# Kernel optimization log

Measured on AMD Instinct MI355X. Metric: run time of the kernel, lower is better.

Reference implementation:

```python
import jax, jax.numpy as jnp
import numpy as np

H = 64            # LSTM hidden size
EH = 2 * H        # encoder output feature dim (bidirectional, 128)
B, T = 512, 512


def setup_inputs() -> dict:
    key = jax.random.key(0)
    ks = jax.random.split(key, 16)
    s = 0.05
    inp = {
        "h0": jax.random.normal(ks[0], (2, B, H), jnp.float32),
        "c0": jax.random.normal(ks[1], (2, B, H), jnp.float32),
        "encoder_outputs": jax.random.normal(ks[2], (B, T, EH), jnp.float32),
        # attn: Linear(4*H=256 -> 1)
        "W_attn": jax.random.normal(ks[3], (1, 4 * H), jnp.float32) * s,
        "b_attn": jax.random.normal(ks[4], (1,), jnp.float32) * s,
        # attn_combine: Linear(256 -> 64)
        "W_comb": jax.random.normal(ks[5], (H, 4 * H), jnp.float32) * s,
        "b_comb": jax.random.normal(ks[6], (H,), jnp.float32) * s,
        # bidirectional LSTM (1 layer), PyTorch gate order i,f,g,o
        "w_ih_f": jax.random.normal(ks[7], (4 * H, H), jnp.float32) * s,
        "w_hh_f": jax.random.normal(ks[8], (4 * H, H), jnp.float32) * s,
        "b_ih_f": jax.random.normal(ks[9], (4 * H,), jnp.float32) * s,
        "b_hh_f": jax.random.normal(ks[10], (4 * H,), jnp.float32) * s,
        "w_ih_r": jax.random.normal(ks[11], (4 * H, H), jnp.float32) * s,
        "w_hh_r": jax.random.normal(ks[12], (4 * H, H), jnp.float32) * s,
        "b_ih_r": jax.random.normal(ks[13], (4 * H,), jnp.float32) * s,
        "b_hh_r": jax.random.normal(ks[14], (4 * H,), jnp.float32) * s,
        "di": 256,
    }
    return inp


def _lstm_cell(x, h, c, w_ih, w_hh, b_ih, b_hh):
    # x,h,c: (b, H); weights: (4H, H). PyTorch gate order: i, f, g, o.
    gates = x @ w_ih.T + b_ih + h @ w_hh.T + b_hh  # (b, 4H)
    i, f, g, o = jnp.split(gates, 4, axis=-1)
    c_new = jax.nn.sigmoid(f) * c + jax.nn.sigmoid(i) * jnp.tanh(g)
    h_new = jax.nn.sigmoid(o) * jnp.tanh(c_new)
    return h_new, c_new


def reference(h0, c0, encoder_outputs, W_attn, b_attn, W_comb, b_comb,
              w_ih_f, w_hh_f, b_ih_f, b_hh_f, w_ih_r, w_hh_r, b_ih_r, b_hh_r, di):
    b, t, h = encoder_outputs.shape
    # hidden[0].view(-1, 128): row-major flatten of (2,b,64) into (b,128)
    dec_hidden = h0.reshape(-1, 2 * H)  # (b, 128)
    hid_rep = jnp.broadcast_to(dec_hidden[:, None, :], (b, t, 2 * H))
    cat = jnp.concatenate([encoder_outputs, hid_rep], axis=2)  # (b,t,256)
    scores = cat @ W_attn.T + b_attn                 # (b,t,1)
    attn_w = jax.nn.softmax(scores, axis=1)          # softmax over time
    # bmm(enc^T (b,h,t), attn_w (b,t,1)) -> (b,h)
    attn_applied = jnp.einsum('bth,bt->bh', encoder_outputs, attn_w[..., 0])
    out = jnp.concatenate([encoder_outputs[:, di, :], attn_applied], axis=1)  # (b,256)
    out = jax.nn.relu(out @ W_comb.T + b_comb)       # (b,64)
    # single-step bidirectional LSTM (seq len 1: both directions see same step)
    h_f, c_f = _lstm_cell(out, h0[0], c0[0], w_ih_f, w_hh_f, b_ih_f, b_hh_f)
    h_r, c_r = _lstm_cell(out, h0[1], c0[1], w_ih_r, w_hh_r, b_ih_r, b_hh_r)
    output = jnp.concatenate([h_f, h_r], axis=-1)[:, None, :]  # (b,1,128)
    h_new = jnp.stack([h_f, h_r], axis=0)  # (2,b,64)
    c_new = jnp.stack([c_f, c_r], axis=0)
    return output, h_new, c_new
```

## Files before the change

kernel.cpp:

```cpp
#include <hip/hip_runtime.h>

#define B_  512
#define T_  512
#define H_  64
#define EH_ 128
#define NW  8
#define NG  32

__device__ __forceinline__ float sigm(float x) { return 1.0f / (1.0f + __expf(-x)); }

__device__ __forceinline__ float dot4(const float4& a, const float4& b) {
  return a.x * b.x + a.y * b.y + a.z * b.z + a.w * b.w;
}
__device__ __forceinline__ float dot8(const float4& a1, const float4& a2,
                                      const float4& b1, const float4& b2) {
  return dot4(a1, b1) + dot4(a2, b2);
}

__global__ __launch_bounds__(512, 4)
void attn_decoder_fused(const float* __restrict__ h0, const float* __restrict__ c0,
                        const float* __restrict__ enc,
                        const float* __restrict__ Wa,  const float* __restrict__ ba,
                        const float* __restrict__ Wc,  const float* __restrict__ bc,
                        const float* __restrict__ wif, const float* __restrict__ whf,
                        const float* __restrict__ bif, const float* __restrict__ bhf,
                        const float* __restrict__ wir, const float* __restrict__ whr,
                        const float* __restrict__ bir, const float* __restrict__ bhr,
                        const int* __restrict__ dip,
                        float* __restrict__ out)
{
  const int b    = blockIdx.x;
  const int tid  = threadIdx.x;
  const int lane = tid & 63;
  const int wv   = tid >> 6;
  const int grp  = lane >> 4;
  const int gl   = lane & 15;

  __shared__ float s_l[NG];
  __shared__ float s_acc[NG][EH_];
  __shared__ float s_cat[2 * EH_];
  __shared__ float s_comb[H_];
  __shared__ float s_h0[2 * H_];
  __shared__ float s_gates[2][4 * H_];

  const float* encb = enc + (size_t)b * T_ * EH_;

  const float4 w1 = *(const float4*)(&Wa[4 * gl]);
  const float4 w2 = *(const float4*)(&Wa[64 + 4 * gl]);

  float  l = 0.0f;
  float4 acc1 = {0.f, 0.f, 0.f, 0.f}, acc2 = {0.f, 0.f, 0.f, 0.f};

  const float* rb = encb + (size_t)(wv * 64 + grp) * EH_ + 4 * gl;

#pragma unroll 1
  for (int it = 0; it < 4; ++it) {
    const float* p0 = rb + (size_t)(it * 16) * EH_;
    float4 eA1 = *(const float4*)(p0);
    float4 eA2 = *(const float4*)(p0 + 64);
    float4 eB1 = *(const float4*)(p0 + 4 * EH_);
    float4 eB2 = *(const float4*)(p0 + 4 * EH_ + 64);
    float4 eC1 = *(const float4*)(p0 + 8 * EH_);
    float4 eC2 = *(const float4*)(p0 + 8 * EH_ + 64);
    float4 eD1 = *(const float4*)(p0 + 12 * EH_);
    float4 eD2 = *(const float4*)(p0 + 12 * EH_ + 64);

    float sA = dot8(eA1, eA2, w1, w2);
    float sB = dot8(eB1, eB2, w1, w2);
    float sC = dot8(eC1, eC2, w1, w2);
    float sD = dot8(eD1, eD2, w1, w2);
#pragma unroll
    for (int off = 8; off; off >>= 1) {
      sA += __shfl_xor(sA, off, 64);
      sB += __shfl_xor(sB, off, 64);
      sC += __shfl_xor(sC, off, 64);
      sD += __shfl_xor(sD, off, 64);
    }
    float pA = __expf(sA), pB = __expf(sB);
    float pC = __expf(sC), pD = __expf(sD);
    l += pA + pB + pC + pD;
    acc1.x += pA * eA1.x + pB * eB1.x + pC * eC1.x + pD * eD1.x;
    acc1.y += pA * eA1.y + pB * eB1.y + pC * eC1.y + pD * eD1.y;
    acc1.z += pA * eA1.z + pB * eB1.z + pC * eC1.z + pD * eD1.z;
    acc1.w += pA * eA1.w + pB * eB1.w + pC * eC1.w + pD * eD1.w;
    acc2.x += pA * eA2.x + pB * eB2.x + pC * eC2.x + pD * eD2.x;
    acc2.y += pA * eA2.y + pB * eB2.y + pC * eC2.y + pD * eD2.y;
    acc2.z += pA * eA2.z + pB * eB2.z + pC * eC2.z + pD * eD2.z;
    acc2.w += pA * eA2.w + pB * eB2.w + pC * eC2.w + pD * eD2.w;
  }

  const int g = wv * 4 + grp;
  *(float4*)(&s_acc[g][4 * gl])      = acc1;
  *(float4*)(&s_acc[g][64 + 4 * gl]) = acc2;
  if (gl == 0) s_l[g] = l;
  __syncthreads();

  const int di = dip[0];

  if (tid < EH_) {
    float L = 0.0f, a = 0.0f;
#pragma unroll
    for (int w = 0; w < NG; ++w) { L += s_l[w]; a += s_acc[w][tid]; }
    s_cat[EH_ + tid] = a / L;
    s_cat[tid]       = encb[(size_t)di * EH_ + tid];
  } else if (tid < 2 * EH_) {
    int j = tid - EH_;
    s_h0[j] = h0[(j >> 6) * B_ * H_ + b * H_ + (j & 63)];
  }
  __syncthreads();

  {
    float4 c4 = *(const float4*)(&s_cat[4 * lane]);
#pragma unroll
    for (int batch = 0; batch < 2; ++batch) {
      const int r0 = wv * 8 + batch * 4;
      float sA = dot4(*(const float4*)(Wc + (r0 + 0) * 256 + 4 * lane), c4);
      float sB = dot4(*(const float4*)(Wc + (r0 + 1) * 256 + 4 * lane), c4);
      float sC = dot4(*(const float4*)(Wc + (r0 + 2) * 256 + 4 * lane), c4);
      float sD = dot4(*(const float4*)(Wc + (r0 + 3) * 256 + 4 * lane), c4);
#pragma unroll
      for (int off = 32; off; off >>= 1) {
        sA += __shfl_xor(sA, off, 64);
        sB += __shfl_xor(sB, off, 64);
        sC += __shfl_xor(sC, off, 64);
        sD += __shfl_xor(sD, off, 64);
      }
      if (lane < 4) {
        int r = r0 + lane;
        float v = (lane == 0) ? sA : (lane == 1) ? sB : (lane == 2) ? sC : sD;
        s_comb[r] = fmaxf(v + bc[r], 0.0f);
      }
    }
  }
  __syncthreads();

  {
    const int dir   = wv >> 2;
    const int gbase = (wv & 3) * 64;
    const float* wih = dir ? wir : wif;
    const float* whh = dir ? whr : whf;
    const float* bih = dir ? bir : bif;
    const float* bhh = dir ? bhr : bhf;
    float4 cm4 = *(const float4*)(&s_comb[4 * gl]);
    float4 h4  = *(const float4*)(&s_h0[dir * H_ + 4 * gl]);
#pragma unroll
    for (int batch = 0; batch < 4; ++batch) {
      const int r0 = gbase + batch * 16;
      float sA = dot4(*(const float4*)(wih + (r0 +  0 + grp) * H_ + 4 * gl), cm4)
               + dot4(*(const float4*)(whh + (r0 +  0 + grp) * H_ + 4 * gl), h4);
      float sB = dot4(*(const float4*)(wih + (r0 +  4 + grp) * H_ + 4 * gl), cm4)
               + dot4(*(const float4*)(whh + (r0 +  4 + grp) * H_ + 4 * gl), h4);
      float sC = dot4(*(const float4*)(wih + (r0 +  8 + grp) * H_ + 4 * gl), cm4)
               + dot4(*(const float4*)(whh + (r0 +  8 + grp) * H_ + 4 * gl), h4);
      float sD = dot4(*(const float4*)(wih + (r0 + 12 + grp) * H_ + 4 * gl), cm4)
               + dot4(*(const float4*)(whh + (r0 + 12 + grp) * H_ + 4 * gl), h4);
#pragma unroll
      for (int off = 8; off; off >>= 1) {
        sA += __shfl_xor(sA, off, 64);
        sB += __shfl_xor(sB, off, 64);
        sC += __shfl_xor(sC, off, 64);
        sD += __shfl_xor(sD, off, 64);
      }
      if (gl < 4) {
        int gg = r0 + gl * 4 + grp;
        float v = (gl == 0) ? sA : (gl == 1) ? sB : (gl == 2) ? sC : sD;
        s_gates[dir][gg] = v + bih[gg] + bhh[gg];
      }
    }
  }
  __syncthreads();

  if (tid < 2 * H_) {
    int dir = tid >> 6, j = tid & 63;
    float gi = s_gates[dir][j];
    float gf = s_gates[dir][H_ + j];
    float gg = s_gates[dir][2 * H_ + j];
    float go = s_gates[dir][3 * H_ + j];
    float cp = c0[dir * B_ * H_ + b * H_ + j];
    float cn = sigm(gf) * cp + sigm(gi) * tanhf(gg);
    float hn = sigm(go) * tanhf(cn);
    out[b * 2 * H_ + dir * H_ + j]                    = hn;
    out[B_ * 2 * H_ + dir * B_ * H_ + b * H_ + j]     = hn;
    out[2 * B_ * 2 * H_ + dir * B_ * H_ + b * H_ + j] = cn;
  }
}

extern "C" void kernel_launch(void* const* d_in, const int* in_sizes, int n_in,
                              void* d_out, int out_size, void* d_ws, size_t ws_size,
                              hipStream_t stream) {
  const float* h0  = (const float*)d_in[0];
  const float* c0  = (const float*)d_in[1];
  const float* enc = (const float*)d_in[2];
  const float* Wa  = (const float*)d_in[3];
  const float* ba  = (const float*)d_in[4];
  const float* Wc  = (const float*)d_in[5];
  const float* bc  = (const float*)d_in[6];
  const float* wif = (const float*)d_in[7];
  const float* whf = (const float*)d_in[8];
  const float* bif = (const float*)d_in[9];
  const float* bhf = (const float*)d_in[10];
  const float* wir = (const float*)d_in[11];
  const float* whr = (const float*)d_in[12];
  const float* bir = (const float*)d_in[13];
  const float* bhr = (const float*)d_in[14];
  const int*   dip = (const int*)d_in[15];
  float* out = (float*)d_out;

  attn_decoder_fused<<<B_, 512, 0, stream>>>(h0, c0, enc, Wa, ba, Wc, bc,
                                             wif, whf, bif, bhf,
                                             wir, whr, bir, bhr, dip, out);
}
```

Before: 34.06 us.

## Split attention reduction across two blocks per batch with separate epilogue kernel

Splits the fused kernel in two. The first kernel launches two blocks per batch row, each covering half of the time steps and writing its partial weighted sums and softmax denominator to workspace. A second kernel combines the two partials and runs the combine layer and the LSTM cells. The goal is more parallelism, with 1024 blocks instead of 512 for the memory-bound encoder sweep and a lighter per-block working set. The cost is a second launch, a workspace round-trip, and extra loads of the LSTM weights.

```diff
diff --git a/kernel.cpp b/kernel.cpp
--- a/kernel.cpp
+++ b/kernel.cpp
@@ -4,8 +4,8 @@
 #define T_  512
 #define H_  64
 #define EH_ 128
-#define NW  8
 #define NG  32
+#define WS_STRIDE 132
 
 __device__ __forceinline__ float sigm(float x) { return 1.0f / (1.0f + __expf(-x)); }
 
@@ -17,19 +17,13 @@
   return dot4(a1, b1) + dot4(a2, b2);
 }
 
-__global__ __launch_bounds__(512, 4)
-void attn_decoder_fused(const float* __restrict__ h0, const float* __restrict__ c0,
-                        const float* __restrict__ enc,
-                        const float* __restrict__ Wa,  const float* __restrict__ ba,
-                        const float* __restrict__ Wc,  const float* __restrict__ bc,
-                        const float* __restrict__ wif, const float* __restrict__ whf,
-                        const float* __restrict__ bif, const float* __restrict__ bhf,
-                        const float* __restrict__ wir, const float* __restrict__ whr,
-                        const float* __restrict__ bir, const float* __restrict__ bhr,
-                        const int* __restrict__ dip,
-                        float* __restrict__ out)
+__global__ __launch_bounds__(512, 8)
+void attn_partial(const float* __restrict__ enc, const float* __restrict__ Wa,
+                  float* __restrict__ ws)
 {
-  const int b    = blockIdx.x;
+  const int bid  = blockIdx.x;
+  const int b    = bid >> 1;
+  const int sp   = bid & 1;
   const int tid  = threadIdx.x;
   const int lane = tid & 63;
   const int wv   = tid >> 6;
@@ -38,10 +32,6 @@
 
   __shared__ float s_l[NG];
   __shared__ float s_acc[NG][EH_];
-  __shared__ float s_cat[2 * EH_];
-  __shared__ float s_comb[H_];
-  __shared__ float s_h0[2 * H_];
-  __shared__ float s_gates[2][4 * H_];
 
   const float* encb = enc + (size_t)b * T_ * EH_;
 
@@ -51,10 +41,10 @@
   float  l = 0.0f;
   float4 acc1 = {0.f, 0.f, 0.f, 0.f}, acc2 = {0.f, 0.f, 0.f, 0.f};
 
-  const float* rb = encb + (size_t)(wv * 64 + grp) * EH_ + 4 * gl;
+  const float* rb = encb + (size_t)(sp * 256 + wv * 32 + grp) * EH_ + 4 * gl;
 
 #pragma unroll 1
-  for (int it = 0; it < 4; ++it) {
+  for (int it = 0; it < 2; ++it) {
     const float* p0 = rb + (size_t)(it * 16) * EH_;
     float4 eA1 = *(const float4*)(p0);
     float4 eA2 = *(const float4*)(p0 + 64);
@@ -95,14 +85,53 @@
   if (gl == 0) s_l[g] = l;
   __syncthreads();
 
+  float* wsp = ws + (size_t)bid * WS_STRIDE;
+  if (tid < EH_) {
+    float a = 0.0f;
+#pragma unroll
+    for (int w = 0; w < NG; ++w) a += s_acc[w][tid];
+    wsp[tid] = a;
+    if (tid == 0) {
+      float L = 0.0f;
+#pragma unroll
+      for (int w = 0; w < NG; ++w) L += s_l[w];
+      wsp[EH_] = L;
+    }
+  }
+}
+
+__global__ __launch_bounds__(512, 4)
+void attn_epilogue(const float* __restrict__ h0, const float* __restrict__ c0,
+                   const float* __restrict__ enc,
+                   const float* __restrict__ Wc,  const float* __restrict__ bc,
+                   const float* __restrict__ wif, const float* __restrict__ whf,
+                   const float* __restrict__ bif, const float* __restrict__ bhf,
+                   const float* __restrict__ wir, const float* __restrict__ whr,
+                   const float* __restrict__ bir, const float* __restrict__ bhr,
+                   const int* __restrict__ dip,
+                   const float* __restrict__ ws,
+                   float* __restrict__ out)
+{
+  const int b    = blockIdx.x;
+  const int tid  = threadIdx.x;
+  const int lane = tid & 63;
+  const int wv   = tid >> 6;
+  const int grp  = lane >> 4;
+  const int gl   = lane & 15;
+
+  __shared__ float s_cat[2 * EH_];
+  __shared__ float s_comb[H_];
+  __shared__ float s_h0[2 * H_];
+  __shared__ float s_gates[2][4 * H_];
+
   const int di = dip[0];
+  const float* w0 = ws + (size_t)(2 * b) * WS_STRIDE;
+  const float* w1p = ws + (size_t)(2 * b + 1) * WS_STRIDE;
 
   if (tid < EH_) {
-    float L = 0.0f, a = 0.0f;
-#pragma unroll
-    for (int w = 0; w < NG; ++w) { L += s_l[w]; a += s_acc[w][tid]; }
-    s_cat[EH_ + tid] = a / L;
-    s_cat[tid]       = encb[(size_t)di * EH_ + tid];
+    float L = w0[EH_] + w1p[EH_];
+    s_cat[EH_ + tid] = (w0[tid] + w1p[tid]) / L;
+    s_cat[tid]       = enc[((size_t)b * T_ + di) * EH_ + tid];
   } else if (tid < 2 * EH_) {
     int j = tid - EH_;
     s_h0[j] = h0[(j >> 6) * B_ * H_ + b * H_ + (j & 63)];
@@ -192,7 +221,6 @@
   const float* c0  = (const float*)d_in[1];
   const float* enc = (const float*)d_in[2];
   const float* Wa  = (const float*)d_in[3];
-  const float* ba  = (const float*)d_in[4];
   const float* Wc  = (const float*)d_in[5];
   const float* bc  = (const float*)d_in[6];
   const float* wif = (const float*)d_in[7];
@@ -205,8 +233,10 @@
   const float* bhr = (const float*)d_in[14];
   const int*   dip = (const int*)d_in[15];
   float* out = (float*)d_out;
-
-  attn_decoder_fused<<<B_, 512, 0, stream>>>(h0, c0, enc, Wa, ba, Wc, bc,
-                                             wif, whf, bif, bhf,
-                                             wir, whr, bir, bhr, dip, out);
-}
+  float* ws  = (float*)d_ws;
+
+  attn_partial<<<2 * B_, 512, 0, stream>>>(enc, Wa, ws);
+  attn_epilogue<<<B_, 512, 0, stream>>>(h0, (const float*)d_in[1], enc, Wc, bc,
+                                        wif, whf, bif, bhf,
+                                        wir, whr, bir, bhr, dip, ws, out);
+}
```

After: 37.09 us. 1.09x slower.
